# Kernel tuning notes

Hardware: AMD Instinct MI355X
Metric: run time of the kernel (lower is better)

The kernel has to match this reference:

```python
import jax, jax.numpy as jnp
import numpy as np

B = 2
Z, Y, X = 21, 256, 256          # spatial_shape (z, y, x)
OZ, OY, OX = 10, 128, 128       # strided conv output grid: floor((in+2p-3)/2)+1
CIN, C1, C2 = 16, 32, 64
N = 400_000
EPS = 1e-3                      # BN eps from norm_cfg


def setup_inputs() -> dict:
    rng = np.random.default_rng(0)
    total = B * Z * Y * X
    lin = rng.choice(total, size=N, replace=False)
    lin.sort()
    b = (lin // (Z * Y * X)).astype(np.int64)
    r = lin % (Z * Y * X)
    z = r // (Y * X)
    r = r % (Y * X)
    y = r // X
    x = r % X
    coors = np.stack([b, z, y, x], axis=1).astype(np.int32)

    # Active output coords of SparseConv3d(k=3, s=2, pad=[0,1,1]):
    # input c is seen by output o iff o*2 - p + j == c for some j in {0,1,2}.
    pads = (0, 1, 1)
    cand_dims = []
    for c, p, osz in zip((z, y, x), pads, (OZ, OY, OX)):
        per = []
        for j in range(3):
            num = c + p - j
            o = num // 2
            valid = (num % 2 == 0) & (num >= 0) & (o < osz)
            per.append((o, valid))
        cand_dims.append(per)
    cand = []
    for oz, vz in cand_dims[0]:
        for oy, vy in cand_dims[1]:
            for ox, vx in cand_dims[2]:
                v = vz & vy & vx
                if v.any():
                    cand.append(np.stack([b[v], oz[v], oy[v], ox[v]], axis=1))
    out_coors = np.unique(np.concatenate(cand, axis=0), axis=0).astype(np.int32)

    key = jax.random.key(0)
    ks = jax.random.split(key, 11)
    voxel_feat = jax.random.normal(ks[0], (N, CIN), jnp.float32)
    W1 = jax.random.normal(ks[1], (27, CIN, C1), jnp.float32) / np.float32(np.sqrt(27 * CIN))
    W2 = jax.random.normal(ks[2], (27, C1, C2), jnp.float32) / np.float32(np.sqrt(27 * C1))
    g1 = 1.0 + 0.1 * jax.random.normal(ks[3], (C1,), jnp.float32)
    b1 = 0.1 * jax.random.normal(ks[4], (C1,), jnp.float32)
    m1 = 0.1 * jax.random.normal(ks[5], (C1,), jnp.float32)
    v1 = 0.5 + jnp.abs(jax.random.normal(ks[6], (C1,), jnp.float32)) * 0.5
    g2 = 1.0 + 0.1 * jax.random.normal(ks[7], (C2,), jnp.float32)
    b2 = 0.1 * jax.random.normal(ks[8], (C2,), jnp.float32)
    m2 = 0.1 * jax.random.normal(ks[9], (C2,), jnp.float32)
    v2 = 0.5 + jnp.abs(jax.random.normal(ks[10], (C2,), jnp.float32)) * 0.5
    return {
        "voxel_feat": voxel_feat,
        "coors": jnp.asarray(coors),
        "out_coors": jnp.asarray(out_coors),
        "W1": W1, "g1": g1, "b1": b1, "m1": m1, "v1": v1,
        "W2": W2, "g2": g2, "b2": b2, "m2": m2, "v2": v2,
        "batch_size": B,
    }


def _bn_relu(x, g, b, m, v):
    return jax.nn.relu((x - m) * (g * jax.lax.rsqrt(v + EPS)) + b)


def _build_grid(coors, n):
    # dense hash of active voxels -> row index (rulebook lookup table)
    lin = ((coors[:, 0] * Z + coors[:, 1]) * Y + coors[:, 2]) * X + coors[:, 3]
    return jnp.full((B * Z * Y * X,), -1, jnp.int32).at[lin].set(jnp.arange(n, dtype=jnp.int32))


def _sparse_conv(feat, grid, bcol, zz, yy, xx, W, cout):
    # gather-GEMM-scatter for one kernel offset set; loop over 27 offsets is structural
    n = zz[0].shape[0]
    out = jnp.zeros((n, cout), feat.dtype)
    for k in range(27):
        z_, y_, x_ = zz[k], yy[k], xx[k]
        ok = (z_ >= 0) & (z_ < Z) & (y_ >= 0) & (y_ < Y) & (x_ >= 0) & (x_ < X)
        l = ((bcol * Z + jnp.clip(z_, 0, Z - 1)) * Y + jnp.clip(y_, 0, Y - 1)) * X + jnp.clip(x_, 0, X - 1)
        idx = grid[l]
        ok = ok & (idx >= 0)
        f = feat[jnp.where(ok, idx, 0)]
        out = out + jnp.where(ok[:, None], f @ W[k], jnp.zeros((), feat.dtype))
    return out


def reference(voxel_feat, coors, out_coors, W1, g1, b1, m1, v1, W2, g2, b2, m2, v2, batch_size):
    n = voxel_feat.shape[0]
    grid = _build_grid(coors, n)

    # --- SubMConv3d(k=3, pad=1): out[c] = sum_j W1[j] @ in[c + j - 1], outputs only at input sites
    zz, yy, xx = [], [], []
    for dz in (-1, 0, 1):
        for dy in (-1, 0, 1):
            for dx in (-1, 0, 1):
                zz.append(coors[:, 1] + dz)
                yy.append(coors[:, 2] + dy)
                xx.append(coors[:, 3] + dx)
    f1 = _bn_relu(_sparse_conv(voxel_feat, grid, coors[:, 0], zz, yy, xx, W1, C1), g1, b1, m1, v1)

    # --- SparseConv3d(k=3, s=2, pad=[0,1,1]): input coord = o*2 - p + j
    zz, yy, xx = [], [], []
    for jz in range(3):
        for jy in range(3):
            for jx in range(3):
                zz.append(out_coors[:, 1] * 2 - 0 + jz)
                yy.append(out_coors[:, 2] * 2 - 1 + jy)
                xx.append(out_coors[:, 3] * 2 - 1 + jx)
    f2 = _bn_relu(_sparse_conv(f1, grid, out_coors[:, 0], zz, yy, xx, W2, C2), g2, b2, m2, v2)

    return f2, out_coors, batch_size
```

## Files before the change

kernel.cpp:

```cpp
#include <hip/hip_runtime.h>

#define ZD 21
#define YD 256
#define XD 256
#define BD 2
#define NCIN 16
#define NC1 32
#define NC2 64
#define BN_EPS 1e-3f

#define ZP 23
#define YP 258
#define XP 258
#define YPXP 66564
#define GRID_TOT (BD * ZP * YPXP)
#define TAILN 133647

typedef __attribute__((ext_vector_type(8))) short short8;
typedef __attribute__((ext_vector_type(4))) float floatx4;

__constant__ int KOFF[28] = {
    0, 1, 2, 258, 259, 260, 516, 517, 518,
    66564, 66565, 66566, 66822, 66823, 66824, 67080, 67081, 67082,
    133128, 133129, 133130, 133386, 133387, 133388, 133644, 133645, 133646,
    0};

__device__ inline unsigned short rne_bf16(float w) {
    unsigned b = __float_as_uint(w);
    return (unsigned short)((b + 0x7FFFu + ((b >> 16) & 1u)) >> 16);
}

__global__ __launch_bounds__(256) void prep_k(
    const float* __restrict__ feat, const int* __restrict__ coors,
    const float* __restrict__ W1, const float* __restrict__ W2,
    const int* __restrict__ oc, const int* __restrict__ bs,
    int* __restrict__ grid, unsigned short* __restrict__ featb,
    unsigned short* __restrict__ f1,
    short* __restrict__ wp1, short* __restrict__ wp2,
    float* __restrict__ out2, int n, int m4) {
    const int i = blockIdx.x * 256 + threadIdx.x;

    if (i < n) {
        const int4 c = ((const int4*)coors)[i];
        grid[((c.x * ZP + c.y + 1) * YP + c.z + 1) * XP + c.w + 1] = i + 1;
    }
    if (i < 2 * n) {
        const float4* p = (const float4*)feat + (size_t)i * 2;
        const float4 a = p[0], b = p[1];
        short8 o;
        o[0] = (short)rne_bf16(a.x); o[1] = (short)rne_bf16(a.y);
        o[2] = (short)rne_bf16(a.z); o[3] = (short)rne_bf16(a.w);
        o[4] = (short)rne_bf16(b.x); o[5] = (short)rne_bf16(b.y);
        o[6] = (short)rne_bf16(b.z); o[7] = (short)rne_bf16(b.w);
        ((short8*)featb)[i + 2] = o;
    }
    if (i < 2) ((short8*)featb)[i] = (short8)0;
    if (i < 4) ((short8*)f1)[i] = (short8)0;
    if (i < 14 * 2 * 512) {
        int pair = i / 1024, r = i % 1024, cb = r / 512, e = r % 512;
        int lane = e / 8, j = e % 8, kk = (lane >> 4) * 8 + j;
        int ko = pair * 2 + (kk >> 4), ci = kk & 15, co = cb * 16 + (lane & 15);
        float w = (ko < 27) ? W1[(ko * NCIN + ci) * NC1 + co] : 0.f;
        wp1[(pair * 2 + cb) * 512 + e] = (short)rne_bf16(w);
    }
    const int t2 = i - 14 * 2 * 512;
    if (t2 >= 0 && t2 < 27 * 4 * 512) {
        int k = t2 / 2048, r = t2 % 2048, cb = r / 512, e = r % 512;
        int lane = e / 8, j = e % 8, ci = (lane >> 4) * 8 + j, co = cb * 16 + (lane & 15);
        wp2[(k * 4 + cb) * 512 + e] = (short)rne_bf16(W2[(k * NC1 + ci) * NC2 + co]);
    }
    if (i < m4) out2[i] = (float)oc[i];
    if (i == m4) out2[m4] = (float)bs[0];
}

__global__ __launch_bounds__(256, 4) void conv1_k(
    const unsigned short* __restrict__ featb, const int* __restrict__ coors,
    const short* __restrict__ wp1,
    const float* __restrict__ g1, const float* __restrict__ b1,
    const float* __restrict__ m1, const float* __restrict__ v1,
    const int* __restrict__ gridp, unsigned short* __restrict__ f1, int n, int tail0) {
    const int tid = threadIdx.x;
    const int lane = tid & 63;
    const int quad = lane >> 4;
    const int mrow = lane & 15;
    const int vbase = blockIdx.x * 128 + (tid >> 6) * 32;
    const int ko_add = quad >> 1;
    const int ci_half = quad & 1;

    __shared__ short lw[2][1024];

    int pb[2];
#pragma unroll
    for (int mt = 0; mt < 2; ++mt) {
        const int v = vbase + mt * 16 + mrow;
        if (v < n) {
            const int4 cc = ((const int4*)coors)[v];
            pb[mt] = ((cc.x * ZP + cc.y) * YP + cc.z) * XP + cc.w;
        } else {
            pb[mt] = tail0;
        }
    }

    floatx4 d[2][2];
#pragma unroll
    for (int mt = 0; mt < 2; ++mt)
#pragma unroll
        for (int cb = 0; cb < 2; ++cb) d[mt][cb] = (floatx4){0.f, 0.f, 0.f, 0.f};

    const short8* __restrict__ wg = (const short8*)wp1;

    if (tid < 128) ((short8*)lw[0])[tid] = wg[tid];
    int id_c[2], id_n[2];
    {
        const int koff = KOFF[ko_add];
#pragma unroll
        for (int mt = 0; mt < 2; ++mt) id_c[mt] = gridp[pb[mt] + koff];
    }
    {
        const int koff = KOFF[2 + ko_add];
#pragma unroll
        for (int mt = 0; mt < 2; ++mt) id_n[mt] = gridp[pb[mt] + koff];
    }
    short8 a_c[2];
#pragma unroll
    for (int mt = 0; mt < 2; ++mt)
        a_c[mt] = *(const short8*)(featb + (unsigned)(id_c[mt] * NCIN + ci_half * 8));
    __syncthreads();

    int buf = 0;
#pragma unroll 1
    for (int pair = 0; pair < 14; ++pair) {
        const int kst = (pair < 13) ? pair + 1 : 13;
        short8 wreg;
        if (tid < 128) wreg = wg[kst * 128 + tid];

        short8 wf0 = ((const short8*)lw[buf])[0 * 64 + lane];
        short8 wf1 = ((const short8*)lw[buf])[1 * 64 + lane];

        short8 a_nx[2];
#pragma unroll
        for (int mt = 0; mt < 2; ++mt)
            a_nx[mt] = *(const short8*)(featb + (unsigned)(id_n[mt] * NCIN + ci_half * 8));

        int id_f[2];
        {
            const int kbase = (pair < 12) ? (pair + 2) * 2 : 26;
            const int koff = KOFF[kbase + ko_add];
#pragma unroll
            for (int mt = 0; mt < 2; ++mt) id_f[mt] = gridp[pb[mt] + koff];
        }

#pragma unroll
        for (int mt = 0; mt < 2; ++mt) {
            d[mt][0] = __builtin_amdgcn_mfma_f32_16x16x32_bf16(a_c[mt], wf0, d[mt][0], 0, 0, 0);
            d[mt][1] = __builtin_amdgcn_mfma_f32_16x16x32_bf16(a_c[mt], wf1, d[mt][1], 0, 0, 0);
        }

        if (tid < 128) ((short8*)lw[buf ^ 1])[tid] = wreg;
        __syncthreads();

#pragma unroll
        for (int mt = 0; mt < 2; ++mt) {
            a_c[mt] = a_nx[mt]; id_c[mt] = id_n[mt]; id_n[mt] = id_f[mt];
        }
        buf ^= 1;
    }

    const int col = lane & 15;
#pragma unroll
    for (int cb = 0; cb < 2; ++cb) {
        const int ch = cb * 16 + col;
        const float sc = g1[ch] * rsqrtf(v1[ch] + BN_EPS);
        const float sb = b1[ch] - m1[ch] * sc;
#pragma unroll
        for (int mt = 0; mt < 2; ++mt) {
#pragma unroll
            for (int r = 0; r < 4; ++r) {
                const int v = vbase + mt * 16 + quad * 4 + r;
                if (v < n) {
                    const float o = fmaxf(fmaf(d[mt][cb][r], sc, sb), 0.f);
                    f1[(unsigned)((v + 1) * NC1 + ch)] = rne_bf16(o);
                }
            }
        }
    }
}

__global__ __launch_bounds__(256, 4) void conv2_k(
    const unsigned short* __restrict__ f1,
    const int* __restrict__ ocoors, const short* __restrict__ wp2,
    const float* __restrict__ g2, const float* __restrict__ b2,
    const float* __restrict__ m2, const float* __restrict__ v2,
    const int* __restrict__ gridp, float* __restrict__ out, int m, int tail0) {
    const int tid = threadIdx.x;
    const int lane = tid & 63;
    const int quad = lane >> 4;
    const int mrow = lane & 15;
    const int vbase = blockIdx.x * 128 + (tid >> 6) * 32;

    __shared__ short lw[2][2048];

    int pb[2];
#pragma unroll
    for (int mt = 0; mt < 2; ++mt) {
        const int v = vbase + mt * 16 + mrow;
        if (v < m) {
            const int4 cc = ((const int4*)ocoors)[v];
            pb[mt] = ((cc.x * ZP + 2 * cc.y + 1) * YP + 2 * cc.z) * XP + 2 * cc.w;
        } else {
            pb[mt] = tail0;
        }
    }

    floatx4 d[2][4];
#pragma unroll
    for (int mt = 0; mt < 2; ++mt)
#pragma unroll
        for (int cb = 0; cb < 4; ++cb) d[mt][cb] = (floatx4){0.f, 0.f, 0.f, 0.f};

    const short8* __restrict__ wg = (const short8*)wp2;

    ((short8*)lw[0])[tid] = wg[tid];
    int id_c[2], id_n[2];
#pragma unroll
    for (int mt = 0; mt < 2; ++mt) id_c[mt] = gridp[pb[mt] + KOFF[0]];
#pragma unroll
    for (int mt = 0; mt < 2; ++mt) id_n[mt] = gridp[pb[mt] + KOFF[1]];
    short8 a_c[2];
#pragma unroll
    for (int mt = 0; mt < 2; ++mt)
        a_c[mt] = *(const short8*)(f1 + (unsigned)(id_c[mt] * NC1 + quad * 8));
    __syncthreads();

    int buf = 0;
#pragma unroll 1
    for (int k = 0; k < 27; ++k) {
        const int kst = (k < 26) ? k + 1 : 26;
        short8 wreg = wg[kst * 256 + tid];

        short8 wf[4];
#pragma unroll
        for (int cb = 0; cb < 4; ++cb)
            wf[cb] = ((const short8*)lw[buf])[cb * 64 + lane];

        short8 a_nx[2];
#pragma unroll
        for (int mt = 0; mt < 2; ++mt)
            a_nx[mt] = *(const short8*)(f1 + (unsigned)(id_n[mt] * NC1 + quad * 8));

        int id_f[2];
        {
            const int koff = KOFF[(k < 25) ? k + 2 : 26];
#pragma unroll
            for (int mt = 0; mt < 2; ++mt) id_f[mt] = gridp[pb[mt] + koff];
        }

#pragma unroll
        for (int mt = 0; mt < 2; ++mt) {
#pragma unroll
            for (int cb = 0; cb < 4; ++cb)
                d[mt][cb] = __builtin_amdgcn_mfma_f32_16x16x32_bf16(a_c[mt], wf[cb], d[mt][cb], 0, 0, 0);
        }

        ((short8*)lw[buf ^ 1])[tid] = wreg;
        __syncthreads();

#pragma unroll
        for (int mt = 0; mt < 2; ++mt) {
            a_c[mt] = a_nx[mt]; id_c[mt] = id_n[mt]; id_n[mt] = id_f[mt];
        }
        buf ^= 1;
    }

    const int col = lane & 15;
#pragma unroll
    for (int cb = 0; cb < 4; ++cb) {
        const int ch = cb * 16 + col;
        const float sc = g2[ch] * rsqrtf(v2[ch] + BN_EPS);
        const float sb = b2[ch] - m2[ch] * sc;
#pragma unroll
        for (int mt = 0; mt < 2; ++mt) {
#pragma unroll
            for (int r = 0; r < 4; ++r) {
                const int v = vbase + mt * 16 + quad * 4 + r;
                if (v < m)
                    out[(unsigned)(v * NC2 + ch)] = fmaxf(fmaf(d[mt][cb][r], sc, sb), 0.f);
            }
        }
    }
}

extern "C" void kernel_launch(void* const* d_in, const int* in_sizes, int n_in,
                              void* d_out, int out_size, void* d_ws, size_t ws_size,
                              hipStream_t stream) {
    const float* feat  = (const float*)d_in[0];
    const int*   coors = (const int*)d_in[1];
    const int*   ocoors= (const int*)d_in[2];
    const float* W1 = (const float*)d_in[3];
    const float* g1 = (const float*)d_in[4];
    const float* b1 = (const float*)d_in[5];
    const float* m1 = (const float*)d_in[6];
    const float* v1 = (const float*)d_in[7];
    const float* W2 = (const float*)d_in[8];
    const float* g2 = (const float*)d_in[9];
    const float* b2 = (const float*)d_in[10];
    const float* m2 = (const float*)d_in[11];
    const float* v2 = (const float*)d_in[12];
    const int*   bs = (const int*)d_in[13];

    const int n = in_sizes[0] / NCIN;
    const int m = in_sizes[2] / 4;

    char* ws = (char*)d_ws;
    int* grid = (int*)ws;
    size_t off = ((size_t)(GRID_TOT + TAILN) * sizeof(int) + 255) & ~(size_t)255;
    unsigned short* featb = (unsigned short*)(ws + off);
    off += ((size_t)(n + 1) * NCIN * 2 + 255) & ~(size_t)255;
    unsigned short* f1 = (unsigned short*)(ws + off);
    off += ((size_t)(n + 1) * NC1 * 2 + 255) & ~(size_t)255;
    short* wp1 = (short*)(ws + off);
    off += (14 * 2 * 512 * 2 + 255) & ~(size_t)255;
    short* wp2 = (short*)(ws + off);

    float* out = (float*)d_out;
    float* out2 = out + (size_t)m * NC2;

    int prep_threads = 2 * n;
    if (m * 4 + 1 > prep_threads) prep_threads = m * 4 + 1;

    hipMemsetAsync(grid, 0x00, (size_t)(GRID_TOT + TAILN) * sizeof(int), stream);
    prep_k<<<(prep_threads + 255) / 256, 256, 0, stream>>>(feat, coors, W1, W2, ocoors, bs,
                                                           grid, featb, f1, wp1, wp2, out2, n, m * 4);

    conv1_k<<<(n + 127) / 128, 256, 0, stream>>>(featb, coors, wp1, g1, b1, m1, v1,
                                                 grid, f1, n, GRID_TOT);

    conv2_k<<<(m + 127) / 128, 256, 0, stream>>>(f1, ocoors, wp2,
                                                 g2, b2, m2, v2, grid, out, m, GRID_TOT);
}
```

Baseline: 236.1 us.

## Drop LDS weight staging and deepen gather prefetch pipeline in sparse convs

Both conv kernels stop staging weights through double-buffered shared memory with a per-iteration __syncthreads, and instead load weight fragments directly from global memory (cache-resident) per lane. The gather pipeline is deepened: grid indices are fetched three steps ahead and features two steps ahead, with KOFF padded so lookahead past the end reads valid offsets. This removes block-wide barriers and LDS traffic in exchange for more global/L1 weight loads and higher register pressure.

Result: slower. 265.0 us (+12.3%).

```diff
diff --git a/kernel.cpp b/kernel.cpp
--- a/kernel.cpp
+++ b/kernel.cpp
@@ -19,11 +19,11 @@
 typedef __attribute__((ext_vector_type(8))) short short8;
 typedef __attribute__((ext_vector_type(4))) float floatx4;
 
-__constant__ int KOFF[28] = {
+__constant__ int KOFF[40] = {
     0, 1, 2, 258, 259, 260, 516, 517, 518,
     66564, 66565, 66566, 66822, 66823, 66824, 67080, 67081, 67082,
     133128, 133129, 133130, 133386, 133387, 133388, 133644, 133645, 133646,
-    0};
+    0, 0, 0, 0, 0, 0, 0, 0, 0, 0, 0, 0, 0};
 
 __device__ inline unsigned short rne_bf16(float w) {
     unsigned b = __float_as_uint(w);
@@ -87,8 +87,6 @@
     const int ko_add = quad >> 1;
     const int ci_half = quad & 1;
 
-    __shared__ short lw[2][1024];
-
     int pb[2];
 #pragma unroll
     for (int mt = 0; mt < 2; ++mt) {
@@ -109,61 +107,51 @@
 
     const short8* __restrict__ wg = (const short8*)wp1;
 
-    if (tid < 128) ((short8*)lw[0])[tid] = wg[tid];
-    int id_c[2], id_n[2];
-    {
-        const int koff = KOFF[ko_add];
-#pragma unroll
-        for (int mt = 0; mt < 2; ++mt) id_c[mt] = gridp[pb[mt] + koff];
-    }
-    {
-        const int koff = KOFF[2 + ko_add];
-#pragma unroll
-        for (int mt = 0; mt < 2; ++mt) id_n[mt] = gridp[pb[mt] + koff];
-    }
-    short8 a_c[2];
-#pragma unroll
-    for (int mt = 0; mt < 2; ++mt)
-        a_c[mt] = *(const short8*)(featb + (unsigned)(id_c[mt] * NCIN + ci_half * 8));
-    __syncthreads();
-
-    int buf = 0;
+    int ia[2], ib[2], i2[2], i3[2];
+#pragma unroll
+    for (int mt = 0; mt < 2; ++mt) ia[mt] = gridp[pb[mt] + KOFF[0 + ko_add]];
+#pragma unroll
+    for (int mt = 0; mt < 2; ++mt) ib[mt] = gridp[pb[mt] + KOFF[2 + ko_add]];
+#pragma unroll
+    for (int mt = 0; mt < 2; ++mt) i2[mt] = gridp[pb[mt] + KOFF[4 + ko_add]];
+#pragma unroll
+    for (int mt = 0; mt < 2; ++mt) i3[mt] = gridp[pb[mt] + KOFF[6 + ko_add]];
+    short8 a0[2], a1[2];
+#pragma unroll
+    for (int mt = 0; mt < 2; ++mt)
+        a0[mt] = *(const short8*)(featb + (unsigned)(ia[mt] * NCIN + ci_half * 8));
+#pragma unroll
+    for (int mt = 0; mt < 2; ++mt)
+        a1[mt] = *(const short8*)(featb + (unsigned)(ib[mt] * NCIN + ci_half * 8));
+
 #pragma unroll 1
     for (int pair = 0; pair < 14; ++pair) {
-        const int kst = (pair < 13) ? pair + 1 : 13;
-        short8 wreg;
-        if (tid < 128) wreg = wg[kst * 128 + tid];
-
-        short8 wf0 = ((const short8*)lw[buf])[0 * 64 + lane];
-        short8 wf1 = ((const short8*)lw[buf])[1 * 64 + lane];
-
-        short8 a_nx[2];
+        const short8 wf0 = wg[(pair * 2 + 0) * 64 + lane];
+        const short8 wf1 = wg[(pair * 2 + 1) * 64 + lane];
+
+        short8 a2[2];
 #pragma unroll
         for (int mt = 0; mt < 2; ++mt)
-            a_nx[mt] = *(const short8*)(featb + (unsigned)(id_n[mt] * NCIN + ci_half * 8));
-
-        int id_f[2];
+            a2[mt] = *(const short8*)(featb + (unsigned)(i2[mt] * NCIN + ci_half * 8));
+
+        int i4[2];
         {
-            const int kbase = (pair < 12) ? (pair + 2) * 2 : 26;
-            const int koff = KOFF[kbase + ko_add];
-#pragma unroll
-            for (int mt = 0; mt < 2; ++mt) id_f[mt] = gridp[pb[mt] + koff];
-        }
-
-#pragma unroll
-        for (int mt = 0; mt < 2; ++mt) {
-            d[mt][0] = __builtin_amdgcn_mfma_f32_16x16x32_bf16(a_c[mt], wf0, d[mt][0], 0, 0, 0);
-            d[mt][1] = __builtin_amdgcn_mfma_f32_16x16x32_bf16(a_c[mt], wf1, d[mt][1], 0, 0, 0);
-        }
-
-        if (tid < 128) ((short8*)lw[buf ^ 1])[tid] = wreg;
-        __syncthreads();
-
-#pragma unroll
-        for (int mt = 0; mt < 2; ++mt) {
-            a_c[mt] = a_nx[mt]; id_c[mt] = id_n[mt]; id_n[mt] = id_f[mt];
-        }
-        buf ^= 1;
+            const int koff = KOFF[2 * (pair + 4) + ko_add];
+#pragma unroll
+            for (int mt = 0; mt < 2; ++mt) i4[mt] = gridp[pb[mt] + koff];
+        }
+
+#pragma unroll
+        for (int mt = 0; mt < 2; ++mt) {
+            d[mt][0] = __builtin_amdgcn_mfma_f32_16x16x32_bf16(a0[mt], wf0, d[mt][0], 0, 0, 0);
+            d[mt][1] = __builtin_amdgcn_mfma_f32_16x16x32_bf16(a0[mt], wf1, d[mt][1], 0, 0, 0);
+        }
+
+#pragma unroll
+        for (int mt = 0; mt < 2; ++mt) {
+            a0[mt] = a1[mt]; a1[mt] = a2[mt];
+            i2[mt] = i3[mt]; i3[mt] = i4[mt];
+        }
     }
 
     const int col = lane & 15;
@@ -198,8 +186,6 @@
     const int mrow = lane & 15;
     const int vbase = blockIdx.x * 128 + (tid >> 6) * 32;
 
-    __shared__ short lw[2][2048];
-
     int pb[2];
 #pragma unroll
     for (int mt = 0; mt < 2; ++mt) {
@@ -220,56 +206,54 @@
 
     const short8* __restrict__ wg = (const short8*)wp2;
 
-    ((short8*)lw[0])[tid] = wg[tid];
-    int id_c[2], id_n[2];
-#pragma unroll
-    for (int mt = 0; mt < 2; ++mt) id_c[mt] = gridp[pb[mt] + KOFF[0]];
-#pragma unroll
-    for (int mt = 0; mt < 2; ++mt) id_n[mt] = gridp[pb[mt] + KOFF[1]];
-    short8 a_c[2];
-#pragma unroll
-    for (int mt = 0; mt < 2; ++mt)
-        a_c[mt] = *(const short8*)(f1 + (unsigned)(id_c[mt] * NC1 + quad * 8));
-    __syncthreads();
-
-    int buf = 0;
+    int ia[2], ib[2], i2[2], i3[2];
+#pragma unroll
+    for (int mt = 0; mt < 2; ++mt) ia[mt] = gridp[pb[mt] + KOFF[0]];
+#pragma unroll
+    for (int mt = 0; mt < 2; ++mt) ib[mt] = gridp[pb[mt] + KOFF[1]];
+#pragma unroll
+    for (int mt = 0; mt < 2; ++mt) i2[mt] = gridp[pb[mt] + KOFF[2]];
+#pragma unroll
+    for (int mt = 0; mt < 2; ++mt) i3[mt] = gridp[pb[mt] + KOFF[3]];
+    short8 a0[2], a1[2];
+#pragma unroll
+    for (int mt = 0; mt < 2; ++mt)
+        a0[mt] = *(const short8*)(f1 + (unsigned)(ia[mt] * NC1 + quad * 8));
+#pragma unroll
+    for (int mt = 0; mt < 2; ++mt)
+        a1[mt] = *(const short8*)(f1 + (unsigned)(ib[mt] * NC1 + quad * 8));
+
 #pragma unroll 1
     for (int k = 0; k < 27; ++k) {
-        const int kst = (k < 26) ? k + 1 : 26;
-        short8 wreg = wg[kst * 256 + tid];
-
         short8 wf[4];
 #pragma unroll
         for (int cb = 0; cb < 4; ++cb)
-            wf[cb] = ((const short8*)lw[buf])[cb * 64 + lane];
-
-        short8 a_nx[2];
+            wf[cb] = wg[(k * 4 + cb) * 64 + lane];
+
+        short8 a2[2];
 #pragma unroll
         for (int mt = 0; mt < 2; ++mt)
-            a_nx[mt] = *(const short8*)(f1 + (unsigned)(id_n[mt] * NC1 + quad * 8));
-
-        int id_f[2];
+            a2[mt] = *(const short8*)(f1 + (unsigned)(i2[mt] * NC1 + quad * 8));
+
+        int i4[2];
         {
-            const int koff = KOFF[(k < 25) ? k + 2 : 26];
-#pragma unroll
-            for (int mt = 0; mt < 2; ++mt) id_f[mt] = gridp[pb[mt] + koff];
+            const int koff = KOFF[k + 4];
+#pragma unroll
+            for (int mt = 0; mt < 2; ++mt) i4[mt] = gridp[pb[mt] + koff];
         }
 
 #pragma unroll
         for (int mt = 0; mt < 2; ++mt) {
 #pragma unroll
             for (int cb = 0; cb < 4; ++cb)
-                d[mt][cb] = __builtin_amdgcn_mfma_f32_16x16x32_bf16(a_c[mt], wf[cb], d[mt][cb], 0, 0, 0);
-        }
-
-        ((short8*)lw[buf ^ 1])[tid] = wreg;
-        __syncthreads();
-
-#pragma unroll
-        for (int mt = 0; mt < 2; ++mt) {
-            a_c[mt] = a_nx[mt]; id_c[mt] = id_n[mt]; id_n[mt] = id_f[mt];
-        }
-        buf ^= 1;
+                d[mt][cb] = __builtin_amdgcn_mfma_f32_16x16x32_bf16(a0[mt], wf[cb], d[mt][cb], 0, 0, 0);
+        }
+
+#pragma unroll
+        for (int mt = 0; mt < 2; ++mt) {
+            a0[mt] = a1[mt]; a1[mt] = a2[mt];
+            i2[mt] = i3[mt]; i3[mt] = i4[mt];
+        }
     }
 
     const int col = lane & 15;
```
